# Performance work log

Hardware: AMD Instinct MI355X
Metric: run time of the kernel (lower is better)

## Reference

```python
import jax, jax.numpy as jnp
import numpy as np

N_NODES = 50000
N_EDGES = 800000
NODE_DIM = 64
EDGE_DIM = 16
HID = 64
HEADS = 4
LAYERS = 3
N_GRAPHS = 32
N_QUERY = 4096
BN_EPS = 1e-5
LRELU_SLOPE = 0.2


def setup_inputs() -> dict:
    key = jax.random.key(0)
    ks = jax.random.split(key, 20)
    s = 0.1  # weight scale
    return {
        "node_feat": jax.random.normal(ks[0], (N_NODES, NODE_DIM), jnp.float32),
        "edge_feat": jax.random.normal(ks[1], (N_EDGES, EDGE_DIM), jnp.float32),
        "node_proj_w": jax.random.normal(ks[2], (NODE_DIM, HID), jnp.float32) * s,
        "node_proj_b": jax.random.normal(ks[3], (HID,), jnp.float32) * s,
        "edge_proj_w": jax.random.normal(ks[4], (EDGE_DIM, HID), jnp.float32) * s,
        "edge_proj_b": jax.random.normal(ks[5], (HID,), jnp.float32) * s,
        "fc_w": jax.random.normal(ks[6], (LAYERS, HID, HEADS * HID), jnp.float32) * s,
        "fc_edge_w": jax.random.normal(ks[7], (LAYERS, HID, HEADS * HID), jnp.float32) * s,
        "attn_l": jax.random.normal(ks[8], (LAYERS, HEADS, HID), jnp.float32) * s,
        "attn_r": jax.random.normal(ks[9], (LAYERS, HEADS, HID), jnp.float32) * s,
        "attn_e": jax.random.normal(ks[10], (LAYERS, HEADS, HID), jnp.float32) * s,
        "conv_bias": jax.random.normal(ks[11], (LAYERS, HEADS * HID), jnp.float32) * s,
        "bn_gamma": jnp.ones((LAYERS, HID), jnp.float32),
        "bn_beta": jnp.zeros((LAYERS, HID), jnp.float32),
        "head_w": jax.random.normal(ks[12], (HEADS * HID, HID), jnp.float32) * s,
        "head_b": jax.random.normal(ks[13], (HID,), jnp.float32) * s,
        "src": jax.random.randint(ks[14], (N_EDGES,), 0, N_NODES, jnp.int64 if jax.config.jax_enable_x64 else jnp.int32),
        "dst": jax.random.randint(ks[15], (N_EDGES,), 0, N_NODES, jnp.int64 if jax.config.jax_enable_x64 else jnp.int32),
        "graph_ids": jnp.sort(jax.random.randint(ks[16], (N_NODES,), 0, N_GRAPHS)),
        "nodes_idx": jax.random.randint(ks[17], (N_QUERY,), 0, N_NODES),
        "num_graphs": N_GRAPHS,
    }


def reference(node_feat, edge_feat, node_proj_w, node_proj_b, edge_proj_w,
              edge_proj_b, fc_w, fc_edge_w, attn_l, attn_r, attn_e, conv_bias,
              bn_gamma, bn_beta, head_w, head_b, src, dst, graph_ids,
              nodes_idx, num_graphs):
    N = node_feat.shape[0]
    L, H, D = attn_l.shape

    nodes = node_feat @ node_proj_w + node_proj_b        # (N, hid)
    edges = edge_feat @ edge_proj_w + edge_proj_b        # (E, hid)

    x = None
    for l in range(L):
        # NOTE: faithful to original -- every layer consumes the ORIGINAL
        # projected node features (output is never fed back into `nodes`).
        ft = (nodes @ fc_w[l]).reshape(N, H, D)          # (N, H, D)
        fe = (edges @ fc_edge_w[l]).reshape(-1, H, D)    # (E, H, D)
        el = jnp.einsum('nhd,hd->nh', ft, attn_l[l])     # (N, H)
        er = jnp.einsum('nhd,hd->nh', ft, attn_r[l])
        ee = jnp.einsum('ehd,hd->eh', fe, attn_e[l])     # (E, H)
        e = jax.nn.leaky_relu(el[src] + er[dst] + ee, LRELU_SLOPE)
        # edge softmax over incoming edges of each destination node
        emax = jax.ops.segment_max(e, dst, num_segments=N)
        ex = jnp.exp(e - emax[dst])
        denom = jax.ops.segment_sum(ex, dst, num_segments=N)
        a = ex / denom[dst]                              # (E, H)
        # message = a * (feat_src + feat_edge), scatter-sum to dst
        m = a[:, :, None] * (ft[src] + fe)               # (E, H, D)
        rst = jax.ops.segment_sum(m, dst, num_segments=N)  # (N, H, D)
        rst = jax.nn.silu(rst + conv_bias[l].reshape(H, D))
        # BatchNorm1d(hidden) after permute(0,2,1): channel dim is D,
        # stats over (N, H). Training-mode batch statistics.
        mean = rst.mean(axis=(0, 1))
        var = rst.var(axis=(0, 1))
        x = (rst - mean) * jax.lax.rsqrt(var + BN_EPS) * bn_gamma[l] + bn_beta[l]

    x = x.reshape(N, H * D) @ head_w + head_b            # (N, hid)

    ones = jnp.ones((N, 1), x.dtype)
    sums = jax.ops.segment_sum(x, graph_ids, num_segments=num_graphs)
    counts = jax.ops.segment_sum(ones, graph_ids, num_segments=num_graphs)
    pooled = sums / jnp.maximum(counts, 1.0)             # (G, hid)
    return pooled, x[nodes_idx]
```

## Files before the change

kernel.cpp:

```cpp
#include <hip/hip_runtime.h>
#include <cstdint>
#include <cstddef>

#define N_NODES 50000
#define N_EDGES 800000
#define HID 64
#define HEADS 4
#define N_GRAPHS 32
#define N_QUERY 4096
#define N_TILES 3125
#define N_CBLK  391

typedef unsigned short ushort_t;
typedef unsigned int uint_t;
typedef __attribute__((ext_vector_type(8))) short short8_t;
typedef __attribute__((ext_vector_type(4))) float f32x4_t;

__device__ __forceinline__ float b2f(ushort_t h) { return __uint_as_float(((uint_t)h) << 16); }
__device__ __forceinline__ ushort_t f2b(float f) {
    uint_t u = __float_as_uint(f);
    uint_t r = (u + 0x7FFFu + ((u >> 16) & 1u)) >> 16;
    return (ushort_t)r;
}

static constexpr size_t OFF_DEG   = 0;
static constexpr size_t OFF_GST   = 50016;
static constexpr size_t OFF_OFFS  = 50064;
static constexpr size_t OFF_RANK  = 100080;
static constexpr size_t OFF_AL    = 900080;
static constexpr size_t OFF_AR    = 900336;
static constexpr size_t OFF_B     = 900592;
static constexpr size_t OFF_CE    = 900656;
static constexpr size_t OFF_CB    = 900672;
static constexpr size_t OFF_SS    = 900928;
static constexpr size_t OFF_HB2   = 901056;
static constexpr size_t OFF_WQE   = 901120;
static constexpr size_t OFF_WCVT  = 905216;
static constexpr size_t OFF_WHT   = 946176;
static constexpr size_t OFF_EL    = 954368;
static constexpr size_t OFF_ER    = 1154368;
static constexpr size_t OFF_NB    = 1354368;
static constexpr size_t OFF_REC   = 2954368;
static constexpr size_t OFF_U     = 6154624;
static constexpr size_t OFF_RST   = 14154624;
static constexpr size_t OFF_X     = 20554624;
static constexpr size_t OFF_SCR   = 23754624;
static constexpr size_t OFF_SCR2  = 23854720;
static constexpr size_t WS_TOTAL  = 23871104;

__global__ void setup1_kernel(const float* __restrict__ fcw2, const float* __restrict__ fcew2,
                              const float* __restrict__ attl2, const float* __restrict__ attr2,
                              const float* __restrict__ atte2,
                              const float* __restrict__ wpe, const float* __restrict__ bpe,
                              const int* __restrict__ gids,
                              float* __restrict__ Al, float* __restrict__ Ar,
                              float* __restrict__ B, float* __restrict__ Ce,
                              float* __restrict__ Cb, float* __restrict__ Wqe,
                              int* __restrict__ gstart)
{
    int b = blockIdx.x, tid = threadIdx.x;
    if (b == 0) {
        __shared__ float AE[256];
        int c = tid >> 2, h = tid & 3;
        float al = 0.f, ar = 0.f, ae = 0.f;
        for (int d = 0; d < 64; d++) {
            float wl = fcw2[c*256 + h*64 + d];
            float we = fcew2[c*256 + h*64 + d];
            al = fmaf(wl, attl2[h*64 + d], al);
            ar = fmaf(wl, attr2[h*64 + d], ar);
            ae = fmaf(we, atte2[h*64 + d], ae);
        }
        Al[c*4 + h] = al;
        Ar[c*4 + h] = ar;
        AE[c*4 + h] = ae;
        __syncthreads();
        if (tid < 64) {
            int kk = tid >> 2, hh = tid & 3;
            float bb = 0.f;
            for (int d = 0; d < 64; d++) bb = fmaf(wpe[kk*64 + d], AE[d*4 + hh], bb);
            B[kk*4 + hh] = bb;
        }
        if (tid < 4) {
            float ce = 0.f;
            for (int d = 0; d < 64; d++) ce = fmaf(bpe[d], AE[d*4 + tid], ce);
            Ce[tid] = ce;
        }
        {
            float cb = 0.f;
            for (int d = 0; d < 64; d++) cb = fmaf(bpe[d], fcew2[d*256 + tid], cb);
            Cb[tid] = cb;
        }
    } else if (b <= 16) {
        int idx = (b - 1) * 256 + tid;
        int hh = idx >> 10, rem = idx & 1023, kk = rem >> 6, cc = rem & 63;
        float w = 0.f;
        for (int d = 0; d < 64; d++) w = fmaf(wpe[kk*64 + d], fcew2[d*256 + hh*64 + cc], w);
        Wqe[idx] = w;
    } else {
        int g = tid;
        if (g <= N_GRAPHS) {
            int lo = 0, hi = N_NODES;
            while (lo < hi) { int mid = (lo + hi) >> 1; if (gids[mid] < g) lo = mid + 1; else hi = mid; }
            gstart[g] = lo;
        }
    }
}

__global__ void wcvt_kernel(const float* __restrict__ fcw2, const float* __restrict__ Wqe,
                            ushort_t* __restrict__ wcvt)
{
    int idx = blockIdx.x * 256 + threadIdx.x;
    int kt = idx >> 8, col = idx & 255;
    int hc = col >> 6;
    short8_t v8;
#pragma unroll
    for (int j = 0; j < 8; j++) {
        int k = kt*8 + j;
        float v;
        if (k < 256) {
            v = ((k >> 6) == hc) ? fcw2[(size_t)(k & 63)*256 + col] : 0.f;
        } else {
            int kq = k - 256, hh = kq >> 4;
            v = (hh == hc) ? Wqe[hh*1024 + (kq & 15)*64 + (col & 63)] : 0.f;
        }
        v8[j] = (short)f2b(v);
    }
    *(short8_t*)&wcvt[(size_t)idx*8] = v8;
}

__global__ __launch_bounds__(256) void node_proj_kernel(
    const float* __restrict__ nf, const float* __restrict__ wp, const float* __restrict__ bpn,
    const float* __restrict__ Al, const float* __restrict__ Ar,
    ushort_t* __restrict__ nb, float* __restrict__ el, float* __restrict__ er)
{
    __shared__ float rows[4][64];
    int tid = threadIdx.x, w = tid >> 6, lane = tid & 63;
    int n = blockIdx.x * 4 + w;
    rows[w][lane] = nf[(size_t)n*64 + lane];
    __syncthreads();
    float acc = bpn[lane];
    for (int k = 0; k < 64; k++) acc = fmaf(rows[w][k], wp[k*64 + lane], acc);
    nb[(size_t)n*64 + lane] = f2b(acc);
    float pl[4], pr[4];
#pragma unroll
    for (int h = 0; h < 4; h++) { pl[h] = acc * Al[lane*4 + h]; pr[h] = acc * Ar[lane*4 + h]; }
#pragma unroll
    for (int off = 32; off > 0; off >>= 1) {
#pragma unroll
        for (int h = 0; h < 4; h++) {
            pl[h] += __shfl_xor(pl[h], off, 64);
            pr[h] += __shfl_xor(pr[h], off, 64);
        }
    }
    if (lane == 0) {
#pragma unroll
        for (int h = 0; h < 4; h++) { el[(size_t)n*4 + h] = pl[h]; er[(size_t)n*4 + h] = pr[h]; }
    }
}

__global__ void hist_kernel(const int* __restrict__ dst, int* __restrict__ deg,
                            int* __restrict__ rank)
{
    int e = blockIdx.x * 256 + threadIdx.x;
    if (e < N_EDGES) rank[e] = atomicAdd(&deg[dst[e]], 1);
}

__global__ __launch_bounds__(1024) void prefix_kernel(const int* __restrict__ deg,
                                                      int* __restrict__ offs)
{
    __shared__ int wsum[16];
    __shared__ int carry_s;
    int tid = threadIdx.x, lane = tid & 63, w = tid >> 6;
    if (tid == 0) carry_s = 0;
    __syncthreads();
    for (int base = 0; base < N_NODES; base += 1024) {
        int i = base + tid;
        int v = (i < N_NODES) ? deg[i] : 0;
        int incl = v;
#pragma unroll
        for (int off = 1; off < 64; off <<= 1) {
            int y = __shfl_up(incl, off, 64);
            if (lane >= off) incl += y;
        }
        if (lane == 63) wsum[w] = incl;
        __syncthreads();
        int c0 = carry_s;
        int woff = 0;
#pragma unroll
        for (int k = 0; k < 15; k++) woff += (k < w) ? wsum[k] : 0;
        int ex = c0 + woff + incl - v;
        if (i < N_NODES) offs[i] = ex;
        __syncthreads();
        if (tid == 1023) carry_s = c0 + woff + incl;
        __syncthreads();
    }
    if (tid == 0) offs[N_NODES] = carry_s;
}

__global__ __launch_bounds__(256) void logit_kernel(
    const int* __restrict__ rank, const int* __restrict__ offs,
    const int* __restrict__ src, const int* __restrict__ dst,
    const float* __restrict__ edge_feat, const float* __restrict__ el,
    const float* __restrict__ B, const float* __restrict__ Ce,
    int4* __restrict__ rec)
{
    int e = blockIdx.x * 256 + threadIdx.x;
    if (e >= N_EDGES) return;
    int sn = src[e], dn = dst[e];
    const float4* el4 = (const float4*)el;
    float4 a = el4[sn];
    float l0 = Ce[0] + a.x;
    float l1 = Ce[1] + a.y;
    float l2 = Ce[2] + a.z;
    float l3 = Ce[3] + a.w;
    const float4* ef4 = (const float4*)(edge_feat + (size_t)e * 16);
    float4 e0 = ef4[0], e1 = ef4[1], e2 = ef4[2], e3 = ef4[3];
    float ef[16] = {e0.x,e0.y,e0.z,e0.w, e1.x,e1.y,e1.z,e1.w,
                    e2.x,e2.y,e2.z,e2.w, e3.x,e3.y,e3.z,e3.w};
#pragma unroll
    for (int k = 0; k < 16; k++) {
        float f = ef[k];
        l0 = fmaf(f, B[k*4 + 0], l0);
        l1 = fmaf(f, B[k*4 + 1], l1);
        l2 = fmaf(f, B[k*4 + 2], l2);
        l3 = fmaf(f, B[k*4 + 3], l3);
    }
    int slot = offs[dn] + rank[e];
    uint_t lo01 = (uint_t)f2b(l0) | ((uint_t)f2b(l1) << 16);
    uint_t lo23 = (uint_t)f2b(l2) | ((uint_t)f2b(l3) << 16);
    rec[slot] = make_int4((int)lo01, (int)lo23, sn, e);
}

__global__ __launch_bounds__(256) void accum_kernel(
    const int* __restrict__ offs, const int4* __restrict__ rec,
    const float* __restrict__ er, const float* __restrict__ edge_feat,
    const ushort_t* __restrict__ nb, ushort_t* __restrict__ u)
{
    int tid = threadIdx.x;
    int lane = tid & 63;
    int li = lane & 15;
    int node = blockIdx.x * 16 + (tid >> 6) * 4 + ((lane >> 4) & 3);
    int start = offs[node], end = offs[node + 1];
    int deg = end - start;

    float4 er4 = *(const float4*)&er[(size_t)node*4];
    const int4 Z4 = make_int4(0, 0, 0, 0);
    int4 r0 = (li < deg)      ? rec[start + li]      : Z4;
    int4 r1 = (16 + li < deg) ? rec[start + 16 + li] : Z4;

    float pe0[4], pe1[4];
    {
        float l[4] = { b2f((ushort_t)((uint_t)r0.x & 0xffff)) + er4.x,
                       b2f((ushort_t)((uint_t)r0.x >> 16))    + er4.y,
                       b2f((ushort_t)((uint_t)r0.y & 0xffff)) + er4.z,
                       b2f((ushort_t)((uint_t)r0.y >> 16))    + er4.w };
#pragma unroll
        for (int h = 0; h < 4; h++) {
            float lv = (l[h] > 0.f) ? l[h] : 0.2f * l[h];
            pe0[h] = (li < deg) ? __expf(lv) : 0.f;
        }
    }
    {
        float l[4] = { b2f((ushort_t)((uint_t)r1.x & 0xffff)) + er4.x,
                       b2f((ushort_t)((uint_t)r1.x >> 16))    + er4.y,
                       b2f((ushort_t)((uint_t)r1.y & 0xffff)) + er4.z,
                       b2f((ushort_t)((uint_t)r1.y >> 16))    + er4.w };
#pragma unroll
        for (int h = 0; h < 4; h++) {
            float lv = (l[h] > 0.f) ? l[h] : 0.2f * l[h];
            pe1[h] = (16 + li < deg) ? __expf(lv) : 0.f;
        }
    }
    int sn0 = r0.z, eid0 = r0.w;
    int sn1 = r1.z, eid1 = r1.w;

    int mdeg = deg;
#pragma unroll
    for (int off = 1; off < 64; off <<= 1) mdeg = max(mdeg, __shfl_xor(mdeg, off, 64));
    mdeg = __builtin_amdgcn_readfirstlane(mdeg);

    float z0 = 0.f, z1 = 0.f, z2 = 0.f, z3 = 0.f;
    float t[4][4] = {{0.f}};
    float q[4] = {0.f, 0.f, 0.f, 0.f};
    int grpbase = lane & 48;

#pragma unroll 2
    for (int j = 0; j < mdeg; ++j) {
        bool act = j < deg;
        float a0, a1, a2, a3;
        int sn, eid;
        if (j < 32) {
            float v0 = (j < 16) ? pe0[0] : pe1[0];
            float v1 = (j < 16) ? pe0[1] : pe1[1];
            float v2 = (j < 16) ? pe0[2] : pe1[2];
            float v3 = (j < 16) ? pe0[3] : pe1[3];
            int vs = (j < 16) ? sn0 : sn1;
            int ve = (j < 16) ? eid0 : eid1;
            int sl = grpbase | (j & 15);
            a0 = __shfl(v0, sl, 64);
            a1 = __shfl(v1, sl, 64);
            a2 = __shfl(v2, sl, 64);
            a3 = __shfl(v3, sl, 64);
            sn  = __shfl(vs, sl, 64);
            eid = __shfl(ve, sl, 64);
        } else {
            a0 = a1 = a2 = a3 = 0.f;
            sn = 0; eid = 0;
            if (act) {
                int4 rr = rec[start + j];
                float l0 = b2f((ushort_t)((uint_t)rr.x & 0xffff)) + er4.x;
                float l1 = b2f((ushort_t)((uint_t)rr.x >> 16))    + er4.y;
                float l2 = b2f((ushort_t)((uint_t)rr.y & 0xffff)) + er4.z;
                float l3 = b2f((ushort_t)((uint_t)rr.y >> 16))    + er4.w;
                l0 = (l0 > 0.f) ? l0 : 0.2f * l0;
                l1 = (l1 > 0.f) ? l1 : 0.2f * l1;
                l2 = (l2 > 0.f) ? l2 : 0.2f * l2;
                l3 = (l3 > 0.f) ? l3 : 0.2f * l3;
                a0 = __expf(l0); a1 = __expf(l1); a2 = __expf(l2); a3 = __expf(l3);
                sn = rr.z; eid = rr.w;
            }
        }
        z0 += a0; z1 += a1; z2 += a2; z3 += a3;
        ushort4 nv = *(const ushort4*)&nb[(size_t)sn*64 + li*4];
        float nd0 = b2f(nv.x), nd1 = b2f(nv.y), nd2 = b2f(nv.z), nd3 = b2f(nv.w);
        t[0][0] = fmaf(a0, nd0, t[0][0]); t[0][1] = fmaf(a0, nd1, t[0][1]);
        t[0][2] = fmaf(a0, nd2, t[0][2]); t[0][3] = fmaf(a0, nd3, t[0][3]);
        t[1][0] = fmaf(a1, nd0, t[1][0]); t[1][1] = fmaf(a1, nd1, t[1][1]);
        t[1][2] = fmaf(a1, nd2, t[1][2]); t[1][3] = fmaf(a1, nd3, t[1][3]);
        t[2][0] = fmaf(a2, nd0, t[2][0]); t[2][1] = fmaf(a2, nd1, t[2][1]);
        t[2][2] = fmaf(a2, nd2, t[2][2]); t[2][3] = fmaf(a2, nd3, t[2][3]);
        t[3][0] = fmaf(a3, nd0, t[3][0]); t[3][1] = fmaf(a3, nd1, t[3][1]);
        t[3][2] = fmaf(a3, nd2, t[3][2]); t[3][3] = fmaf(a3, nd3, t[3][3]);
        float efv = edge_feat[(size_t)eid*16 + li];
        q[0] = fmaf(a0, efv, q[0]);
        q[1] = fmaf(a1, efv, q[1]);
        q[2] = fmaf(a2, efv, q[2]);
        q[3] = fmaf(a3, efv, q[3]);
    }

    float zinv[4];
    zinv[0] = (z0 > 0.f) ? 1.f / z0 : 0.f;
    zinv[1] = (z1 > 0.f) ? 1.f / z1 : 0.f;
    zinv[2] = (z2 > 0.f) ? 1.f / z2 : 0.f;
    zinv[3] = (z3 > 0.f) ? 1.f / z3 : 0.f;

    ushort_t* up = u + (size_t)node * 320;
#pragma unroll
    for (int h = 0; h < 4; h++) {
        ushort4 tv;
        tv.x = f2b(t[h][0] * zinv[h]); tv.y = f2b(t[h][1] * zinv[h]);
        tv.z = f2b(t[h][2] * zinv[h]); tv.w = f2b(t[h][3] * zinv[h]);
        *(ushort4*)&up[h*64 + li*4] = tv;
        up[256 + h*16 + li] = f2b(q[h] * zinv[h]);
    }
}

__global__ __launch_bounds__(512) void conv_kernel(
    const ushort_t* __restrict__ u, const ushort_t* __restrict__ wcvt,
    const float* __restrict__ Cb, const float* __restrict__ convb2,
    const int* __restrict__ offs, ushort_t* __restrict__ rst, float* __restrict__ scr)
{
    __shared__ ushort_t Bs[8192];
    __shared__ float red[8][512];
    int tid = threadIdx.x, w = tid >> 6, lane = tid & 63;
    int li = lane & 15, lg = lane >> 4;
    int tile = blockIdx.x * 8 + w;
    bool active = tile < N_TILES;
    int n0 = tile * 16;

    f32x4_t acc[16];
#pragma unroll
    for (int cb = 0; cb < 16; cb++) acc[cb] = (f32x4_t){0.f, 0.f, 0.f, 0.f};
    const ushort_t* urow = active ? (u + (size_t)(n0 + li) * 320 + lg * 8) : u;

    for (int kt = 0; kt < 10; kt++) {
        __syncthreads();
#pragma unroll
        for (int s = 0; s < 2; s++) {
            int i = tid + s*512;
            *(short8_t*)&Bs[(size_t)i*8] =
                *(const short8_t*)(wcvt + ((size_t)kt*1024 + i)*8);
        }
        __syncthreads();
        if (active) {
            short8_t a = *(const short8_t*)(urow + kt*32);
#pragma unroll
            for (int half = 0; half < 2; half++) {
                short8_t b[8];
#pragma unroll
                for (int cb = 0; cb < 8; cb++)
                    b[cb] = *(const short8_t*)&Bs[(size_t)(lg*256 + (half*8+cb)*16 + li)*8];
#pragma unroll
                for (int cb = 0; cb < 8; cb++)
                    acc[half*8+cb] = __builtin_amdgcn_mfma_f32_16x16x32_bf16(a, b[cb], acc[half*8+cb], 0, 0, 0);
            }
        }
    }

    if (active) {
        float fl4[4];
#pragma unroll
        for (int j = 0; j < 4; j++) {
            int n = n0 + lg*4 + j;
            fl4[j] = (offs[n+1] > offs[n]) ? 1.f : 0.f;
        }
#pragma unroll
        for (int cb = 0; cb < 16; cb++) {
            int col = cb*16 + li;
            float bias = convb2[col];
            float cbv  = Cb[col];
            float s = 0.f, sq = 0.f;
#pragma unroll
            for (int j = 0; j < 4; j++) {
                float v = acc[cb][j] + bias + fl4[j] * cbv;
                float r = v / (1.f + __expf(-v));
                rst[(size_t)(n0 + lg*4 + j)*256 + col] = f2b(r);
                s += r; sq += r * r;
            }
            s  += __shfl_xor(s, 16, 64);  s  += __shfl_xor(s, 32, 64);
            sq += __shfl_xor(sq, 16, 64); sq += __shfl_xor(sq, 32, 64);
            if (lg == 0) { red[w][col] = s; red[w][256 + col] = sq; }
        }
    } else {
        for (int i = lane; i < 512; i += 64) red[w][i] = 0.f;
    }
    __syncthreads();
    if (tid < 128) {
        int d = tid & 63, part = tid >> 6;
        float t = 0.f;
#pragma unroll
        for (int w2 = 0; w2 < 8; w2++)
#pragma unroll
            for (int g = 0; g < 4; g++)
                t += red[w2][part*256 + g*64 + d];
        scr[(size_t)blockIdx.x*128 + part*64 + d] = t;
    }
}

__global__ __launch_bounds__(128) void scr_reduce_kernel(const float* __restrict__ scr,
                                                         float* __restrict__ scr2)
{
    int b = blockIdx.x, tid = threadIdx.x;
    float s = 0.f;
    for (int r = b; r < N_CBLK; r += 128) s += scr[(size_t)r*128 + tid];
    scr2[(size_t)b*128 + tid] = s;
}

__global__ void bn_finalize_kernel(const float* __restrict__ scr2, const float* __restrict__ gamma2,
                                   const float* __restrict__ beta2, float* __restrict__ ss)
{
    __shared__ float part[8][128];
    __shared__ float tot[128];
    int j = threadIdx.x & 127, chunk = threadIdx.x >> 7;
    float t = 0.f;
    for (int b = chunk; b < 128; b += 8) t += scr2[(size_t)b*128 + j];
    part[chunk][j] = t;
    __syncthreads();
    if (threadIdx.x < 128) {
        float sgm = 0.f;
        for (int c = 0; c < 8; c++) sgm += part[c][threadIdx.x];
        tot[threadIdx.x] = sgm;
    }
    __syncthreads();
    if (threadIdx.x < 64) {
        float inv = 1.f / (float)(N_NODES * HEADS);
        float mean = tot[threadIdx.x] * inv;
        float var  = tot[64 + threadIdx.x] * inv - mean * mean;
        float sc = gamma2[threadIdx.x] * rsqrtf(var + 1e-5f);
        ss[threadIdx.x]      = sc;
        ss[64 + threadIdx.x] = beta2[threadIdx.x] - mean * sc;
    }
}

__global__ void head_prep_kernel(const float* __restrict__ ss, const float* __restrict__ headw,
                                 const float* __restrict__ headb,
                                 ushort_t* __restrict__ wht, float* __restrict__ hb2)
{
    int b = blockIdx.x, tid = threadIdx.x;
    if (b < 64) {
        int idx = b * 256 + tid;
        int c = idx >> 8, k = idx & 255;
        wht[(size_t)((k >> 3)*64 + c)*8 + (k & 7)] = f2b(ss[k & 63] * headw[(size_t)k*64 + c]);
    } else if (tid < 64) {
        float s = headb[tid];
        for (int k = 0; k < 256; k++) s += ss[64 + (k & 63)] * headw[(size_t)k*64 + tid];
        hb2[tid] = s;
    }
}

__global__ __launch_bounds__(512) void head_kernel(
    const ushort_t* __restrict__ rst, const ushort_t* __restrict__ wht,
    const float* __restrict__ hb2, float* __restrict__ x)
{
    __shared__ ushort_t Bs[16384];
    int tid = threadIdx.x, w = tid >> 6, lane = tid & 63;
    int li = lane & 15, lg = lane >> 4;
    int tile = blockIdx.x * 8 + w;
    bool active = tile < N_TILES;
    int n0 = tile * 16;

#pragma unroll
    for (int s = 0; s < 4; s++) {
        int i = tid + s*512;
        *(short8_t*)&Bs[(size_t)i*8] = *(const short8_t*)(wht + (size_t)i*8);
    }
    __syncthreads();

    if (!active) return;
    f32x4_t acc[4];
#pragma unroll
    for (int cb = 0; cb < 4; cb++) acc[cb] = (f32x4_t){0.f, 0.f, 0.f, 0.f};
    const ushort_t* rrow = rst + (size_t)(n0 + li) * 256 + lg * 8;
#pragma unroll
    for (int kt = 0; kt < 8; kt++) {
        short8_t a = *(const short8_t*)(rrow + kt * 32);
        short8_t b[4];
#pragma unroll
        for (int cb = 0; cb < 4; cb++)
            b[cb] = *(const short8_t*)&Bs[(size_t)((kt*4 + lg)*64 + cb*16 + li)*8];
#pragma unroll
        for (int cb = 0; cb < 4; cb++)
            acc[cb] = __builtin_amdgcn_mfma_f32_16x16x32_bf16(a, b[cb], acc[cb], 0, 0, 0);
    }
#pragma unroll
    for (int cb = 0; cb < 4; cb++) {
        int col = cb*16 + li;
        float hb = hb2[col];
#pragma unroll
        for (int j = 0; j < 4; j++)
            x[(size_t)(n0 + lg*4 + j)*64 + col] = acc[cb][j] + hb;
    }
}

__global__ __launch_bounds__(1024) void pool_kernel(const float* __restrict__ x,
                                                    const int* __restrict__ gstart,
                                                    float* __restrict__ out)
{
    __shared__ float red[16][64];
    int g = blockIdx.x;
    int lane = threadIdx.x & 63, w = threadIdx.x >> 6;
    int s = gstart[g], e = gstart[g + 1];
    float acc = 0.f;
    for (int n = s + w; n < e; n += 16) acc += x[(size_t)n*64 + lane];
    red[w][lane] = acc;
    __syncthreads();
    if (w == 0) {
        float t = 0.f;
#pragma unroll
        for (int k = 0; k < 16; k++) t += red[k][lane];
        float c = (float)(e - s);
        out[(size_t)g*64 + lane] = t / fmaxf(c, 1.f);
    }
}

__global__ void gather_kernel(const float* __restrict__ x, const int* __restrict__ nidx,
                              float* __restrict__ outq)
{
    int i = blockIdx.x * 256 + threadIdx.x;
    if (i < N_QUERY * HID) {
        int q = i >> 6, c = i & 63;
        outq[i] = x[(size_t)nidx[q]*64 + c];
    }
}

extern "C" void kernel_launch(void* const* d_in, const int* in_sizes, int n_in,
                              void* d_out, int out_size, void* d_ws, size_t ws_size,
                              hipStream_t stream)
{
    const float* node_feat   = (const float*)d_in[0];
    const float* edge_feat   = (const float*)d_in[1];
    const float* node_proj_w = (const float*)d_in[2];
    const float* node_proj_b = (const float*)d_in[3];
    const float* edge_proj_w = (const float*)d_in[4];
    const float* edge_proj_b = (const float*)d_in[5];
    const float* fc_w        = (const float*)d_in[6];
    const float* fc_edge_w   = (const float*)d_in[7];
    const float* attn_l      = (const float*)d_in[8];
    const float* attn_r      = (const float*)d_in[9];
    const float* attn_e      = (const float*)d_in[10];
    const float* conv_bias   = (const float*)d_in[11];
    const float* bn_gamma    = (const float*)d_in[12];
    const float* bn_beta     = (const float*)d_in[13];
    const float* head_w      = (const float*)d_in[14];
    const float* head_b      = (const float*)d_in[15];
    const int*   src         = (const int*)d_in[16];
    const int*   dst         = (const int*)d_in[17];
    const int*   gids        = (const int*)d_in[18];
    const int*   nidx        = (const int*)d_in[19];

    if (ws_size < WS_TOTAL * sizeof(float)) return;

    float* ws  = (float*)d_ws;
    float* out = (float*)d_out;

    const int L2 = 2;
    const float* fcw2   = fc_w      + (size_t)L2 * HID * HEADS * HID;
    const float* fcew2  = fc_edge_w + (size_t)L2 * HID * HEADS * HID;
    const float* attl2  = attn_l    + (size_t)L2 * HEADS * HID;
    const float* attr2  = attn_r    + (size_t)L2 * HEADS * HID;
    const float* atte2  = attn_e    + (size_t)L2 * HEADS * HID;
    const float* convb2 = conv_bias + (size_t)L2 * HEADS * HID;
    const float* gamma2 = bn_gamma  + (size_t)L2 * HID;
    const float* beta2  = bn_beta   + (size_t)L2 * HID;

    int*   deg     = (int*)(ws + OFF_DEG);
    int*   gstart  = (int*)(ws + OFF_GST);
    int*   offs    = (int*)(ws + OFF_OFFS);
    int*   rank    = (int*)(ws + OFF_RANK);
    float* Al      = ws + OFF_AL;
    float* Ar      = ws + OFF_AR;
    float* Bm      = ws + OFF_B;
    float* Ce      = ws + OFF_CE;
    float* Cb      = ws + OFF_CB;
    float* ss      = ws + OFF_SS;
    float* hb2     = ws + OFF_HB2;
    float* Wqe     = ws + OFF_WQE;
    ushort_t* wcvt = (ushort_t*)(ws + OFF_WCVT);
    ushort_t* wht  = (ushort_t*)(ws + OFF_WHT);
    float* el      = ws + OFF_EL;
    float* er      = ws + OFF_ER;
    ushort_t* nb   = (ushort_t*)(ws + OFF_NB);
    int4*  rec     = (int4*)(ws + OFF_REC);
    ushort_t* u    = (ushort_t*)(ws + OFF_U);
    ushort_t* rst  = (ushort_t*)(ws + OFF_RST);
    float* x       = ws + OFF_X;
    float* scr     = ws + OFF_SCR;
    float* scr2    = ws + OFF_SCR2;

    hipMemsetAsync(d_ws, 0, N_NODES * sizeof(int), stream);

    setup1_kernel<<<18, 256, 0, stream>>>(fcw2, fcew2, attl2, attr2, atte2,
                                          edge_proj_w, edge_proj_b, gids,
                                          Al, Ar, Bm, Ce, Cb, Wqe, gstart);
    wcvt_kernel<<<40, 256, 0, stream>>>(fcw2, Wqe, wcvt);
    node_proj_kernel<<<N_NODES/4, 256, 0, stream>>>(node_feat, node_proj_w, node_proj_b,
                                                    Al, Ar, nb, el, er);
    hist_kernel<<<(N_EDGES + 255)/256, 256, 0, stream>>>(dst, deg, rank);
    prefix_kernel<<<1, 1024, 0, stream>>>(deg, offs);
    logit_kernel<<<(N_EDGES + 255)/256, 256, 0, stream>>>(rank, offs, src, dst, edge_feat,
                                                          el, Bm, Ce, rec);
    accum_kernel<<<N_NODES/16, 256, 0, stream>>>(offs, rec, er, edge_feat, nb, u);
    conv_kernel<<<N_CBLK, 512, 0, stream>>>(u, wcvt, Cb, convb2, offs, rst, scr);
    scr_reduce_kernel<<<128, 128, 0, stream>>>(scr, scr2);
    bn_finalize_kernel<<<1, 1024, 0, stream>>>(scr2, gamma2, beta2, ss);
    head_prep_kernel<<<65, 256, 0, stream>>>(ss, head_w, head_b, wht, hb2);
    head_kernel<<<N_CBLK, 512, 0, stream>>>(rst, wht, hb2, x);
    pool_kernel<<<N_GRAPHS, 1024, 0, stream>>>(x, gstart, out);
    gather_kernel<<<(N_QUERY*HID + 255)/256, 256, 0, stream>>>(x, nidx, out + N_GRAPHS*HID);
}
```

Before: 283.2 us.

## Read conv weights directly from global memory and write per-tile BN partials

The conv kernel no longer stages the weight slice through shared memory with two barriers per k-step. Each wave now loads its B fragments straight from global/L2 and the k-loop is fully unrolled. Blocks shrink to 4 waves, early-exit replaces the inactive-wave path, and BN partial sums are written per tile instead of being reduced per block in shared memory. This removes LDS traffic and synchronisation, but increases global weight reads and makes the scratch reduction walk 3125 rows instead of 391.

```diff
diff --git a/kernel.cpp b/kernel.cpp
--- a/kernel.cpp
+++ b/kernel.cpp
@@ -9,7 +9,7 @@
 #define N_GRAPHS 32
 #define N_QUERY 4096
 #define N_TILES 3125
-#define N_CBLK  391
+#define N_CBLK  782
 
 typedef unsigned short ushort_t;
 typedef unsigned int uint_t;
@@ -45,8 +45,8 @@
 static constexpr size_t OFF_RST   = 14154624;
 static constexpr size_t OFF_X     = 20554624;
 static constexpr size_t OFF_SCR   = 23754624;
-static constexpr size_t OFF_SCR2  = 23854720;
-static constexpr size_t WS_TOTAL  = 23871104;
+static constexpr size_t OFF_SCR2  = 24154624;
+static constexpr size_t WS_TOTAL  = 24171008;
 
 __global__ void setup1_kernel(const float* __restrict__ fcw2, const float* __restrict__ fcew2,
                               const float* __restrict__ attl2, const float* __restrict__ attr2,
@@ -355,85 +355,69 @@
     }
 }
 
-__global__ __launch_bounds__(512) void conv_kernel(
+__global__ __launch_bounds__(256) void conv_kernel(
     const ushort_t* __restrict__ u, const ushort_t* __restrict__ wcvt,
     const float* __restrict__ Cb, const float* __restrict__ convb2,
     const int* __restrict__ offs, ushort_t* __restrict__ rst, float* __restrict__ scr)
 {
-    __shared__ ushort_t Bs[8192];
-    __shared__ float red[8][512];
-    int tid = threadIdx.x, w = tid >> 6, lane = tid & 63;
+    int tid = threadIdx.x, lane = tid & 63;
     int li = lane & 15, lg = lane >> 4;
-    int tile = blockIdx.x * 8 + w;
-    bool active = tile < N_TILES;
+    int tile = blockIdx.x * 4 + (tid >> 6);
+    if (tile >= N_TILES) return;
     int n0 = tile * 16;
 
     f32x4_t acc[16];
 #pragma unroll
     for (int cb = 0; cb < 16; cb++) acc[cb] = (f32x4_t){0.f, 0.f, 0.f, 0.f};
-    const ushort_t* urow = active ? (u + (size_t)(n0 + li) * 320 + lg * 8) : u;
-
+    const ushort_t* urow = u + (size_t)(n0 + li) * 320 + lg * 8;
+    const ushort_t* wbase = wcvt + ((size_t)lg * 256 + li) * 8;
+
+#pragma unroll
     for (int kt = 0; kt < 10; kt++) {
-        __syncthreads();
-#pragma unroll
-        for (int s = 0; s < 2; s++) {
-            int i = tid + s*512;
-            *(short8_t*)&Bs[(size_t)i*8] =
-                *(const short8_t*)(wcvt + ((size_t)kt*1024 + i)*8);
-        }
-        __syncthreads();
-        if (active) {
-            short8_t a = *(const short8_t*)(urow + kt*32);
-#pragma unroll
-            for (int half = 0; half < 2; half++) {
-                short8_t b[8];
-#pragma unroll
-                for (int cb = 0; cb < 8; cb++)
-                    b[cb] = *(const short8_t*)&Bs[(size_t)(lg*256 + (half*8+cb)*16 + li)*8];
-#pragma unroll
-                for (int cb = 0; cb < 8; cb++)
-                    acc[half*8+cb] = __builtin_amdgcn_mfma_f32_16x16x32_bf16(a, b[cb], acc[half*8+cb], 0, 0, 0);
-            }
-        }
-    }
-
-    if (active) {
-        float fl4[4];
+        short8_t a = *(const short8_t*)(urow + kt * 32);
+        const ushort_t* wk = wbase + (size_t)kt * 8192;
+        short8_t b[16];
+#pragma unroll
+        for (int cb = 0; cb < 16; cb++)
+            b[cb] = *(const short8_t*)(wk + (size_t)cb * 128);
+#pragma unroll
+        for (int cb = 0; cb < 16; cb++)
+            acc[cb] = __builtin_amdgcn_mfma_f32_16x16x32_bf16(a, b[cb], acc[cb], 0, 0, 0);
+    }
+
+    float fl4[4];
+#pragma unroll
+    for (int j = 0; j < 4; j++) {
+        int n = n0 + lg*4 + j;
+        fl4[j] = (offs[n+1] > offs[n]) ? 1.f : 0.f;
+    }
+    float ds[4] = {0.f, 0.f, 0.f, 0.f};
+    float dsq[4] = {0.f, 0.f, 0.f, 0.f};
+#pragma unroll
+    for (int cb = 0; cb < 16; cb++) {
+        int col = cb*16 + li;
+        float bias = convb2[col];
+        float cbv  = Cb[col];
+        float s = 0.f, sq = 0.f;
 #pragma unroll
         for (int j = 0; j < 4; j++) {
-            int n = n0 + lg*4 + j;
-            fl4[j] = (offs[n+1] > offs[n]) ? 1.f : 0.f;
-        }
-#pragma unroll
-        for (int cb = 0; cb < 16; cb++) {
-            int col = cb*16 + li;
-            float bias = convb2[col];
-            float cbv  = Cb[col];
-            float s = 0.f, sq = 0.f;
-#pragma unroll
-            for (int j = 0; j < 4; j++) {
-                float v = acc[cb][j] + bias + fl4[j] * cbv;
-                float r = v / (1.f + __expf(-v));
-                rst[(size_t)(n0 + lg*4 + j)*256 + col] = f2b(r);
-                s += r; sq += r * r;
-            }
-            s  += __shfl_xor(s, 16, 64);  s  += __shfl_xor(s, 32, 64);
-            sq += __shfl_xor(sq, 16, 64); sq += __shfl_xor(sq, 32, 64);
-            if (lg == 0) { red[w][col] = s; red[w][256 + col] = sq; }
-        }
-    } else {
-        for (int i = lane; i < 512; i += 64) red[w][i] = 0.f;
-    }
-    __syncthreads();
-    if (tid < 128) {
-        int d = tid & 63, part = tid >> 6;
-        float t = 0.f;
-#pragma unroll
-        for (int w2 = 0; w2 < 8; w2++)
-#pragma unroll
-            for (int g = 0; g < 4; g++)
-                t += red[w2][part*256 + g*64 + d];
-        scr[(size_t)blockIdx.x*128 + part*64 + d] = t;
+            float v = acc[cb][j] + bias + fl4[j] * cbv;
+            float r = v / (1.f + __expf(-v));
+            rst[(size_t)(n0 + lg*4 + j)*256 + col] = f2b(r);
+            s += r; sq += r * r;
+        }
+        s  += __shfl_xor(s, 16, 64);  s  += __shfl_xor(s, 32, 64);
+        sq += __shfl_xor(sq, 16, 64); sq += __shfl_xor(sq, 32, 64);
+        ds[cb & 3]  += s;
+        dsq[cb & 3] += sq;
+    }
+    if (lg == 0) {
+        float* sp = scr + (size_t)tile * 128;
+#pragma unroll
+        for (int m = 0; m < 4; m++) {
+            sp[m*16 + li]      = ds[m];
+            sp[64 + m*16 + li] = dsq[m];
+        }
     }
 }
 
@@ -442,7 +426,7 @@
 {
     int b = blockIdx.x, tid = threadIdx.x;
     float s = 0.f;
-    for (int r = b; r < N_CBLK; r += 128) s += scr[(size_t)r*128 + tid];
+    for (int r = b; r < N_TILES; r += 128) s += scr[(size_t)r*128 + tid];
     scr2[(size_t)b*128 + tid] = s;
 }
 
@@ -640,11 +624,11 @@
     logit_kernel<<<(N_EDGES + 255)/256, 256, 0, stream>>>(rank, offs, src, dst, edge_feat,
                                                           el, Bm, Ce, rec);
     accum_kernel<<<N_NODES/16, 256, 0, stream>>>(offs, rec, er, edge_feat, nb, u);
-    conv_kernel<<<N_CBLK, 512, 0, stream>>>(u, wcvt, Cb, convb2, offs, rst, scr);
+    conv_kernel<<<N_CBLK, 256, 0, stream>>>(u, wcvt, Cb, convb2, offs, rst, scr);
     scr_reduce_kernel<<<128, 128, 0, stream>>>(scr, scr2);
     bn_finalize_kernel<<<1, 1024, 0, stream>>>(scr2, gamma2, beta2, ss);
     head_prep_kernel<<<65, 256, 0, stream>>>(ss, head_w, head_b, wht, hb2);
-    head_kernel<<<N_CBLK, 512, 0, stream>>>(rst, wht, hb2, x);
+    head_kernel<<<(N_TILES + 7)/8, 512, 0, stream>>>(rst, wht, hb2, x);
     pool_kernel<<<N_GRAPHS, 1024, 0, stream>>>(x, gstart, out);
     gather_kernel<<<(N_QUERY*HID + 255)/256, 256, 0, stream>>>(x, nidx, out + N_GRAPHS*HID);
 }
```

Measured after the change: 301.2 us. 6.4% more time.
